# Performance work log

Hardware: AMD Instinct MI355X
Metric: run time of the kernel (lower is better)

Reference implementation:

```python
import jax, jax.numpy as jnp
import numpy as np

THETA_BASE = 10000.0


def rope(x):
    # x: [B, S, D], D even. Interleaved-pair rotary embedding.
    B, S, D = x.shape
    pos = jnp.arange(S, dtype=jnp.float32)                       # [S]
    p = jnp.arange(D // 2, dtype=jnp.float32)                    # p-1 in the torch code
    inv_freq = 1.0 / (THETA_BASE ** (2.0 * p / D))               # [D/2]
    theta = pos[:, None] * inv_freq[None, :]                     # [S, D/2]
    sin_t, cos_t = jnp.sin(theta), jnp.cos(theta)
    x1 = x[..., 0::2]                                            # [B, S, D/2]
    x2 = x[..., 1::2]
    r1 = x1 * cos_t - x2 * sin_t
    r2 = x1 * sin_t + x2 * cos_t
    return jnp.stack((r1, r2), axis=-1).reshape(B, S, D)


def setup_inputs() -> dict:
    key = jax.random.key(0)
    k_x, k_q, k_k, k_v = jax.random.split(key, 4)
    B, S, E, DH = 4, 4096, 1024, 64
    x = jax.random.normal(k_x, (B, S, E), dtype=jnp.float32)
    # causal lower-triangular mask (mask==0 positions are disallowed)
    mask = jnp.tril(jnp.ones((S, S), dtype=jnp.int32))
    W_Q = jax.random.uniform(k_q, (E, DH), dtype=jnp.float32)
    W_K = jax.random.uniform(k_k, (E, DH), dtype=jnp.float32)
    W_V = jax.random.uniform(k_v, (E, DH), dtype=jnp.float32)
    return {"x": x, "mask": mask, "W_Q": W_Q, "W_K": W_K, "W_V": W_V}


def reference(x, mask, W_Q, W_K, W_V):
    d_h = W_Q.shape[1]
    Q = x @ W_Q                                                  # [B, S, d_h]
    K = x @ W_K
    V = x @ W_V
    Q, K = rope(Q), rope(K)
    scores = jnp.einsum('bqd,bkd->bqk', Q, K) / jnp.sqrt(jnp.float32(d_h))
    masked = jnp.where(mask == 0, -jnp.inf, scores)              # broadcast [S,S] -> [B,S,S]
    attn = jax.nn.softmax(masked, axis=-1)
    return jnp.einsum('bqk,bkd->bqd', attn, V)
```

## Files before the change

### kernel.cpp

```cpp
#include <hip/hip_runtime.h>

typedef short short8  __attribute__((ext_vector_type(8)));
typedef short short4v __attribute__((ext_vector_type(4)));
typedef float f32x4   __attribute__((ext_vector_type(4)));

#define NB 4
#define NS 4096
#define NE 1024
#define ND 64

__device__ __forceinline__ short f2bf(float f) {
    unsigned u = __builtin_bit_cast(unsigned, f);
    u = (u + 0x7FFFu + ((u >> 16) & 1u)) >> 16;
    return (short)u;
}
__device__ __forceinline__ float bf2f(short s) {
    unsigned u = ((unsigned)(unsigned short)s) << 16;
    return __builtin_bit_cast(float, u);
}

__global__ void prep_wt(const float* __restrict__ WQ, const float* __restrict__ WK,
                        const float* __restrict__ WV,
                        short* __restrict__ wtp_hi, short* __restrict__ wtp_lo) {
    int idx = blockIdx.x * 256 + threadIdx.x;
    if (idx >= 192 * NE) return;
    int n = idx >> 10, k = idx & (NE - 1);
    int sel = n >> 6, d = n & 63;
    const float* W = (sel == 0) ? WQ : (sel == 1 ? WK : WV);
    float v = W[k * ND + d];
    if (sel == 0) v *= 0.125f;
    short hi = f2bf(v);
    short lo = f2bf(v - bf2f(hi));
    int off = ((k >> 5) * 12 + (n >> 4)) * 512 + ((k & 31) >> 3) * 128 + (n & 15) * 8 + (k & 7);
    wtp_hi[off] = hi;
    wtp_lo[off] = lo;
}

__global__ __launch_bounds__(256, 2) void proj_rope(
        const float* __restrict__ x,
        const short* __restrict__ wtp_hi, const short* __restrict__ wtp_lo,
        short* __restrict__ qhi, short* __restrict__ qlo,
        short* __restrict__ khi, short* __restrict__ klo,
        short* __restrict__ vtb) {
    __shared__ short Xh[32 * 64], Xl[32 * 64];
    const int tid = threadIdx.x;
    const int w = tid >> 6, lane = tid & 63;
    const int g = lane >> 4, cl = lane & 15;
    const int rb = blockIdx.x << 5;
    const int c0 = w * 48;

    f32x4 acc[2][3];
    #pragma unroll
    for (int i = 0; i < 2; ++i)
        #pragma unroll
        for (int j = 0; j < 3; ++j) acc[i][j] = (f32x4){0.f, 0.f, 0.f, 0.f};

    const int srow = tid >> 3, skc = tid & 7;
    const float* xs0 = x + (size_t)(rb + srow) * NE + (skc << 3);
    const int swoff = srow * 64 + ((skc ^ (srow & 7)) << 3);

    const short* bph = wtp_hi + (size_t)(c0 >> 4) * 512 + (lane << 3);
    const short* bpl = wtp_lo + (size_t)(c0 >> 4) * 512 + (lane << 3);

    float4 xr0, xr1;
    short8 b0[6], b1[6];

#define LOADXR(kk) { xr0 = *(const float4*)(xs0 + (kk)); \
                     xr1 = *(const float4*)(xs0 + (kk) + 4); }
#define LOADB(Bs, kk) {                                                      \
        const int ko = ((kk) >> 5) * 6144;                                   \
        _Pragma("unroll")                                                    \
        for (int ct = 0; ct < 3; ++ct) {                                     \
            Bs[ct * 2]     = *(const short8*)(bph + ko + ct * 512);          \
            Bs[ct * 2 + 1] = *(const short8*)(bpl + ko + ct * 512);          \
        } }
#define HALF(h, Bs) {                                                        \
        _Pragma("unroll")                                                    \
        for (int rt = 0; rt < 2; ++rt) {                                     \
            const int R = (rt << 4) + cl;                                    \
            const int ro = R * 64 + ((((h) * 4 + g) ^ (R & 7)) << 3);        \
            short8 ah = *(const short8*)(Xh + ro);                           \
            short8 al = *(const short8*)(Xl + ro);                           \
            _Pragma("unroll")                                                \
            for (int ct = 0; ct < 3; ++ct) {                                 \
                acc[rt][ct] = __builtin_amdgcn_mfma_f32_16x16x32_bf16(ah, Bs[ct*2],   acc[rt][ct], 0, 0, 0); \
                acc[rt][ct] = __builtin_amdgcn_mfma_f32_16x16x32_bf16(ah, Bs[ct*2+1], acc[rt][ct], 0, 0, 0); \
                acc[rt][ct] = __builtin_amdgcn_mfma_f32_16x16x32_bf16(al, Bs[ct*2],   acc[rt][ct], 0, 0, 0); \
            }                                                                \
        } }

    LOADXR(0);
    LOADB(b0, 0);

    #pragma unroll 1
    for (int k0 = 0; k0 < NE; k0 += 64) {
        short8 h8, l8;
        {
            float vv[8] = {xr0.x, xr0.y, xr0.z, xr0.w, xr1.x, xr1.y, xr1.z, xr1.w};
            #pragma unroll
            for (int q = 0; q < 8; ++q) {
                short h = f2bf(vv[q]);
                h8[q] = h;
                l8[q] = f2bf(vv[q] - bf2f(h));
            }
        }
        __syncthreads();
        *(short8*)(Xh + swoff) = h8;
        *(short8*)(Xl + swoff) = l8;
        if (k0 + 64 < NE) LOADXR(k0 + 64);
        LOADB(b1, k0 + 32);
        __syncthreads();
        HALF(0, b0);
        if (k0 + 64 < NE) LOADB(b0, k0 + 64);
        HALF(1, b1);
    }
#undef LOADXR
#undef LOADB
#undef HALF

    #pragma unroll
    for (int rt = 0; rt < 2; ++rt) {
        #pragma unroll
        for (int ct = 0; ct < 3; ++ct) {
            int c = c0 + (ct << 4) + cl;
            #pragma unroll
            for (int r = 0; r < 4; ++r) {
                int row = rb + (rt << 4) + (g << 2) + r;
                int s = row & (NS - 1);
                int b = row >> 12;
                float val = acc[rt][ct][r];
                if (c < 128) {
                    int d = c & 63;
                    int p = d >> 1;
                    float freq = exp2f(-(float)p * 0.41524101186091903f);
                    float theta = (float)s * freq;
                    float sn = sinf(theta), cs = cosf(theta);
                    float partner = __shfl_xor(val, 1);
                    float rot = (c & 1) ? fmaf(partner, sn, val * cs)
                                        : fmaf(-partner, sn, val * cs);
                    short hi = f2bf(rot);
                    short lo = f2bf(rot - bf2f(hi));
                    int off = row * ND + d;
                    if (c < 64) { qhi[off] = hi; qlo[off] = lo; }
                    else        { khi[off] = hi; klo[off] = lo; }
                } else {
                    int d = c - 128;
                    vtb[(b << 18) + ((s >> 5) << 11) + (d << 5) + (s & 31)] = f2bf(val);
                }
            }
        }
    }
}

__global__ __launch_bounds__(256) void kv_pack(short* __restrict__ khi,
                                               short* __restrict__ klo,
                                               short* __restrict__ vtb) {
    __shared__ short Xh[2048], Xl[2048], Vl[2048];
    const int tid = threadIdx.x;
    const size_t base = (size_t)blockIdx.x * 2048;
    *(short8*)(Xh + tid * 8) = *(const short8*)(khi + base + tid * 8);
    *(short8*)(Xl + tid * 8) = *(const short8*)(klo + base + tid * 8);
    *(short8*)(Vl + tid * 8) = *(const short8*)(vtb + base + tid * 8);
    __syncthreads();
    const int ci = (tid >> 7) & 1, hf = (tid >> 6) & 1, ln = tid & 63;
    const int srcK = (ci * 16 + (ln & 15)) * 64 + hf * 32 + (ln >> 4) * 8;
    short8 okh = *(const short8*)(Xh + srcK);
    short8 okl = *(const short8*)(Xl + srcK);
    const int dt = (tid >> 6) & 3;
    const int srcV = (dt * 16 + (ln & 15)) * 32 + (ln >> 4) * 8;
    short8 ov = *(const short8*)(Vl + srcV);
    *(short8*)(khi + base + tid * 8) = okh;
    *(short8*)(klo + base + tid * 8) = okl;
    *(short8*)(vtb + base + tid * 8) = ov;
}

__global__ __launch_bounds__(256, 4) void attn_fused(
        const short* __restrict__ qhi, const short* __restrict__ qlo,
        const short* __restrict__ kfph, const short* __restrict__ kfpl,
        const short* __restrict__ vfp, float* __restrict__ outp) {
    __shared__ short Ps[4][16][40];
    __shared__ float Co[4][16][66];
    __shared__ float Cm[4][16], Cls[4][16];
    const int tid = threadIdx.x;
    const int lane = tid & 63, w = tid >> 6;
    const int g = lane >> 4, cl = lane & 15;
    const int bid = blockIdx.x;
    const int b = (bid >> 1) & 3;
    const int t = 255 - (((bid >> 3) << 1) | (bid & 1));
    const int qw = t << 4;
    const int rowb = b << 12;

    short8 qh[2], ql[2];
    #pragma unroll
    for (int ks = 0; ks < 2; ++ks) {
        int off = ((rowb + qw + cl) << 6) + (ks << 5) + (g << 3);
        qh[ks] = *(const short8*)(qhi + off);
        ql[ks] = *(const short8*)(qlo + off);
    }

    f32x4 o[4];
    #pragma unroll
    for (int i = 0; i < 4; ++i) o[i] = (f32x4){0.f, 0.f, 0.f, 0.f};
    float m = -1e38f, lsp = 0.f;

    const int nkv = (t >> 1) + 1;
    const short* kbaseh = kfph + (size_t)(b << 7) * 2048 + (lane << 3);
    const short* kbasel = kfpl + (size_t)(b << 7) * 2048 + (lane << 3);
    const short* vbase  = vfp  + (size_t)(b << 7) * 2048 + (lane << 3);

    short8 kf[2][4];
    short8 vf[4];

#define LOADK(jj) {                                                          \
        _Pragma("unroll")                                                    \
        for (int ci = 0; ci < 2; ++ci) {                                     \
            const short* kh = kbaseh + (jj) * 2048 + ci * 1024;              \
            const short* kl = kbasel + (jj) * 2048 + ci * 1024;              \
            kf[ci][0] = *(const short8*)(kh);                                \
            kf[ci][1] = *(const short8*)(kh + 512);                          \
            kf[ci][2] = *(const short8*)(kl);                                \
            kf[ci][3] = *(const short8*)(kl + 512);                          \
        } }
#define LOADV(jj) {                                                          \
        _Pragma("unroll")                                                    \
        for (int dt = 0; dt < 4; ++dt)                                       \
            vf[dt] = *(const short8*)(vbase + (jj) * 2048 + dt * 512);       \
        }

    if (w < nkv) {
        LOADK(w); LOADV(w);
        #pragma unroll 1
        for (int j = w; j < nkv; j += 4) {
            f32x4 sc[2];
            #pragma unroll
            for (int ci = 0; ci < 2; ++ci) {
                f32x4 s = (f32x4){0.f, 0.f, 0.f, 0.f};
                s = __builtin_amdgcn_mfma_f32_16x16x32_bf16(kf[ci][0], qh[0], s, 0, 0, 0);
                s = __builtin_amdgcn_mfma_f32_16x16x32_bf16(kf[ci][1], qh[1], s, 0, 0, 0);
                s = __builtin_amdgcn_mfma_f32_16x16x32_bf16(kf[ci][0], ql[0], s, 0, 0, 0);
                s = __builtin_amdgcn_mfma_f32_16x16x32_bf16(kf[ci][1], ql[1], s, 0, 0, 0);
                s = __builtin_amdgcn_mfma_f32_16x16x32_bf16(kf[ci][2], qh[0], s, 0, 0, 0);
                s = __builtin_amdgcn_mfma_f32_16x16x32_bf16(kf[ci][3], qh[1], s, 0, 0, 0);
                sc[ci] = s;
            }
            const int jn = j + 4;
            if (jn < nkv) LOADK(jn);

            if (j == nkv - 1) {
                #pragma unroll
                for (int ci = 0; ci < 2; ++ci)
                    #pragma unroll
                    for (int r = 0; r < 4; ++r)
                        if ((j << 5) + (ci << 4) + (g << 2) + r > qw + cl) sc[ci][r] = -1e30f;
            }
            float pm = fmaxf(fmaxf(fmaxf(sc[0][0], sc[0][1]), fmaxf(sc[0][2], sc[0][3])),
                             fmaxf(fmaxf(sc[1][0], sc[1][1]), fmaxf(sc[1][2], sc[1][3])));
            pm = fmaxf(pm, __shfl_xor(pm, 16));
            pm = fmaxf(pm, __shfl_xor(pm, 32));
            const float mo = m;
            m = fmaxf(m, pm);
            const float rs = __expf(mo - m);
            float psum = 0.f;
            #pragma unroll
            for (int ci = 0; ci < 2; ++ci) {
                float p0 = __expf(sc[ci][0] - m), p1 = __expf(sc[ci][1] - m);
                float p2 = __expf(sc[ci][2] - m), p3 = __expf(sc[ci][3] - m);
                psum += (p0 + p1) + (p2 + p3);
                short4v pk;
                pk[0] = f2bf(p0); pk[1] = f2bf(p1); pk[2] = f2bf(p2); pk[3] = f2bf(p3);
                *(short4v*)(&Ps[w][cl][(ci << 4) + (g << 2)]) = pk;
            }
            lsp = lsp * rs + psum;
            if (__any(m > mo)) {
                float rs4[4];
                #pragma unroll
                for (int r = 0; r < 4; ++r) rs4[r] = __shfl(rs, (g << 2) + r);
                #pragma unroll
                for (int dt = 0; dt < 4; ++dt)
                    #pragma unroll
                    for (int r = 0; r < 4; ++r) o[dt][r] *= rs4[r];
            }
            short8 pa = *(short8*)(&Ps[w][cl][g << 3]);
            #pragma unroll
            for (int dt = 0; dt < 4; ++dt)
                o[dt] = __builtin_amdgcn_mfma_f32_16x16x32_bf16(pa, vf[dt], o[dt], 0, 0, 0);
            if (jn < nkv) LOADV(jn);
        }
    }
#undef LOADK
#undef LOADV

    lsp += __shfl_xor(lsp, 16);
    lsp += __shfl_xor(lsp, 32);
    if (g == 0) { Cm[w][cl] = m; Cls[w][cl] = lsp; }
    #pragma unroll
    for (int dt = 0; dt < 4; ++dt)
        #pragma unroll
        for (int r = 0; r < 4; ++r)
            Co[w][(g << 2) + r][(dt << 4) + cl] = o[dt][r];
    __syncthreads();

    if (w == 0) {
        #pragma unroll
        for (int r = 0; r < 4; ++r) {
            const int row = (g << 2) + r;
            float M = fmaxf(fmaxf(Cm[0][row], Cm[1][row]), fmaxf(Cm[2][row], Cm[3][row]));
            float e0 = __expf(Cm[0][row] - M), e1 = __expf(Cm[1][row] - M);
            float e2 = __expf(Cm[2][row] - M), e3 = __expf(Cm[3][row] - M);
            float L = Cls[0][row] * e0 + Cls[1][row] * e1 + Cls[2][row] * e2 + Cls[3][row] * e3;
            float inv = 1.f / L;
            #pragma unroll
            for (int dt = 0; dt < 4; ++dt) {
                int d = (dt << 4) + cl;
                float O = Co[0][row][d] * e0 + Co[1][row][d] * e1
                        + Co[2][row][d] * e2 + Co[3][row][d] * e3;
                outp[(rowb + qw + row) * ND + d] = O * inv;
            }
        }
    }
}

extern "C" void kernel_launch(void* const* d_in, const int* in_sizes, int n_in,
                              void* d_out, int out_size, void* d_ws, size_t ws_size,
                              hipStream_t stream) {
    const float* x  = (const float*)d_in[0];
    const float* WQ = (const float*)d_in[2];
    const float* WK = (const float*)d_in[3];
    const float* WV = (const float*)d_in[4];

    const size_t need = 786432u + 5u * 2097152u;
    if (ws_size < need) return;

    char* ws = (char*)d_ws;
    short* wtph = (short*)(ws);
    short* wtpl = (short*)(ws + 393216);
    short* qhi  = (short*)(ws + 786432);
    short* qlo  = (short*)(ws + 786432 + 1 * 2097152);
    short* khi  = (short*)(ws + 786432 + 2 * 2097152);
    short* klo  = (short*)(ws + 786432 + 3 * 2097152);
    short* vtb  = (short*)(ws + 786432 + 4 * 2097152);

    prep_wt<<<768, 256, 0, stream>>>(WQ, WK, WV, wtph, wtpl);
    proj_rope<<<512, 256, 0, stream>>>(x, wtph, wtpl, qhi, qlo, khi, klo, vtb);
    kv_pack<<<512, 256, 0, stream>>>(khi, klo, vtb);
    attn_fused<<<1024, 256, 0, stream>>>(qhi, qlo, khi, klo, vtb, (float*)d_out);
}
```

Measured before the change: 82.09 us.

## Double-buffer X tile in projection kernel and halve rows per block

The projection kernel now double-buffers the converted X tile in shared memory. The next chunk is converted and stored while the current one feeds the MFMAs, which cuts the barriers per iteration from two to one, implemented as a custom LDS wait plus barrier. Row tile per block drops from 32 to 16, so the grid doubles to 1024 blocks and only half the threads stage X. This trades more parallelism and overlap for less weight reuse per block, so the weight-fragment loads per output row double.

```diff
diff --git a/kernel.cpp b/kernel.cpp
--- a/kernel.cpp
+++ b/kernel.cpp
@@ -18,6 +18,12 @@
     unsigned u = ((unsigned)(unsigned short)s) << 16;
     return __builtin_bit_cast(float, u);
 }
+
+#define LDS_BAR() do {                                               \
+        asm volatile("s_waitcnt lgkmcnt(0)" ::: "memory");           \
+        __builtin_amdgcn_s_barrier();                                \
+        __builtin_amdgcn_sched_barrier(0);                           \
+    } while (0)
 
 __global__ void prep_wt(const float* __restrict__ WQ, const float* __restrict__ WK,
                         const float* __restrict__ WV,
@@ -42,22 +48,20 @@
         short* __restrict__ qhi, short* __restrict__ qlo,
         short* __restrict__ khi, short* __restrict__ klo,
         short* __restrict__ vtb) {
-    __shared__ short Xh[32 * 64], Xl[32 * 64];
+    __shared__ short Xh[2][1024], Xl[2][1024];
     const int tid = threadIdx.x;
     const int w = tid >> 6, lane = tid & 63;
     const int g = lane >> 4, cl = lane & 15;
-    const int rb = blockIdx.x << 5;
+    const int rb = blockIdx.x << 4;
     const int c0 = w * 48;
 
-    f32x4 acc[2][3];
-    #pragma unroll
-    for (int i = 0; i < 2; ++i)
-        #pragma unroll
-        for (int j = 0; j < 3; ++j) acc[i][j] = (f32x4){0.f, 0.f, 0.f, 0.f};
+    f32x4 acc[3];
+    acc[0] = acc[1] = acc[2] = (f32x4){0.f, 0.f, 0.f, 0.f};
 
     const int srow = tid >> 3, skc = tid & 7;
     const float* xs0 = x + (size_t)(rb + srow) * NE + (skc << 3);
     const int swoff = srow * 64 + ((skc ^ (srow & 7)) << 3);
+    const bool stager = (tid < 128);
 
     const short* bph = wtp_hi + (size_t)(c0 >> 4) * 512 + (lane << 3);
     const short* bpl = wtp_lo + (size_t)(c0 >> 4) * 512 + (lane << 3);
@@ -74,79 +78,79 @@
             Bs[ct * 2]     = *(const short8*)(bph + ko + ct * 512);          \
             Bs[ct * 2 + 1] = *(const short8*)(bpl + ko + ct * 512);          \
         } }
-#define HALF(h, Bs) {                                                        \
-        _Pragma("unroll")                                                    \
-        for (int rt = 0; rt < 2; ++rt) {                                     \
-            const int R = (rt << 4) + cl;                                    \
-            const int ro = R * 64 + ((((h) * 4 + g) ^ (R & 7)) << 3);        \
-            short8 ah = *(const short8*)(Xh + ro);                           \
-            short8 al = *(const short8*)(Xl + ro);                           \
-            _Pragma("unroll")                                                \
-            for (int ct = 0; ct < 3; ++ct) {                                 \
-                acc[rt][ct] = __builtin_amdgcn_mfma_f32_16x16x32_bf16(ah, Bs[ct*2],   acc[rt][ct], 0, 0, 0); \
-                acc[rt][ct] = __builtin_amdgcn_mfma_f32_16x16x32_bf16(ah, Bs[ct*2+1], acc[rt][ct], 0, 0, 0); \
-                acc[rt][ct] = __builtin_amdgcn_mfma_f32_16x16x32_bf16(al, Bs[ct*2],   acc[rt][ct], 0, 0, 0); \
-            }                                                                \
+#define CONVW(buf) if (stager) {                                             \
+        float vv[8] = {xr0.x, xr0.y, xr0.z, xr0.w, xr1.x, xr1.y, xr1.z, xr1.w}; \
+        short8 h8, l8;                                                       \
+        _Pragma("unroll")                                                    \
+        for (int q = 0; q < 8; ++q) {                                        \
+            short h = f2bf(vv[q]);                                           \
+            h8[q] = h;                                                       \
+            l8[q] = f2bf(vv[q] - bf2f(h));                                   \
+        }                                                                    \
+        *(short8*)(Xh[buf] + swoff) = h8;                                    \
+        *(short8*)(Xl[buf] + swoff) = l8;                                    \
+    }
+#define HALF(buf, h, Bs) {                                                   \
+        const int ro = cl * 64 + ((((h) * 4 + g) ^ (cl & 7)) << 3);          \
+        short8 ah = *(const short8*)(Xh[buf] + ro);                          \
+        short8 al = *(const short8*)(Xl[buf] + ro);                          \
+        _Pragma("unroll")                                                    \
+        for (int ct = 0; ct < 3; ++ct) {                                     \
+            acc[ct] = __builtin_amdgcn_mfma_f32_16x16x32_bf16(ah, Bs[ct*2],   acc[ct], 0, 0, 0); \
+            acc[ct] = __builtin_amdgcn_mfma_f32_16x16x32_bf16(ah, Bs[ct*2+1], acc[ct], 0, 0, 0); \
+            acc[ct] = __builtin_amdgcn_mfma_f32_16x16x32_bf16(al, Bs[ct*2],   acc[ct], 0, 0, 0); \
         } }
 
-    LOADXR(0);
+    if (stager) LOADXR(0);
+    CONVW(0);
+    if (stager) LOADXR(64);
     LOADB(b0, 0);
+    __syncthreads();
 
     #pragma unroll 1
     for (int k0 = 0; k0 < NE; k0 += 64) {
-        short8 h8, l8;
-        {
-            float vv[8] = {xr0.x, xr0.y, xr0.z, xr0.w, xr1.x, xr1.y, xr1.z, xr1.w};
-            #pragma unroll
-            for (int q = 0; q < 8; ++q) {
-                short h = f2bf(vv[q]);
-                h8[q] = h;
-                l8[q] = f2bf(vv[q] - bf2f(h));
-            }
-        }
-        __syncthreads();
-        *(short8*)(Xh + swoff) = h8;
-        *(short8*)(Xl + swoff) = l8;
-        if (k0 + 64 < NE) LOADXR(k0 + 64);
+        const int cur = (k0 >> 6) & 1, nxt = cur ^ 1;
+        if (k0 + 64 < NE) {
+            CONVW(nxt);
+            if (stager && k0 + 128 < NE) LOADXR(k0 + 128);
+        }
         LOADB(b1, k0 + 32);
-        __syncthreads();
-        HALF(0, b0);
+        HALF(cur, 0, b0);
         if (k0 + 64 < NE) LOADB(b0, k0 + 64);
-        HALF(1, b1);
+        HALF(cur, 1, b1);
+        LDS_BAR();
     }
 #undef LOADXR
 #undef LOADB
+#undef CONVW
 #undef HALF
 
     #pragma unroll
-    for (int rt = 0; rt < 2; ++rt) {
+    for (int ct = 0; ct < 3; ++ct) {
+        int c = c0 + (ct << 4) + cl;
         #pragma unroll
-        for (int ct = 0; ct < 3; ++ct) {
-            int c = c0 + (ct << 4) + cl;
-            #pragma unroll
-            for (int r = 0; r < 4; ++r) {
-                int row = rb + (rt << 4) + (g << 2) + r;
-                int s = row & (NS - 1);
-                int b = row >> 12;
-                float val = acc[rt][ct][r];
-                if (c < 128) {
-                    int d = c & 63;
-                    int p = d >> 1;
-                    float freq = exp2f(-(float)p * 0.41524101186091903f);
-                    float theta = (float)s * freq;
-                    float sn = sinf(theta), cs = cosf(theta);
-                    float partner = __shfl_xor(val, 1);
-                    float rot = (c & 1) ? fmaf(partner, sn, val * cs)
-                                        : fmaf(-partner, sn, val * cs);
-                    short hi = f2bf(rot);
-                    short lo = f2bf(rot - bf2f(hi));
-                    int off = row * ND + d;
-                    if (c < 64) { qhi[off] = hi; qlo[off] = lo; }
-                    else        { khi[off] = hi; klo[off] = lo; }
-                } else {
-                    int d = c - 128;
-                    vtb[(b << 18) + ((s >> 5) << 11) + (d << 5) + (s & 31)] = f2bf(val);
-                }
+        for (int r = 0; r < 4; ++r) {
+            int row = rb + (g << 2) + r;
+            int s = row & (NS - 1);
+            int b = row >> 12;
+            float val = acc[ct][r];
+            if (c < 128) {
+                int d = c & 63;
+                int p = d >> 1;
+                float freq = exp2f(-(float)p * 0.41524101186091903f);
+                float theta = (float)s * freq;
+                float sn = sinf(theta), cs = cosf(theta);
+                float partner = __shfl_xor(val, 1);
+                float rot = (c & 1) ? fmaf(partner, sn, val * cs)
+                                    : fmaf(-partner, sn, val * cs);
+                short hi = f2bf(rot);
+                short lo = f2bf(rot - bf2f(hi));
+                int off = row * ND + d;
+                if (c < 64) { qhi[off] = hi; qlo[off] = lo; }
+                else        { khi[off] = hi; klo[off] = lo; }
+            } else {
+                int d = c - 128;
+                vtb[(b << 18) + ((s >> 5) << 11) + (d << 5) + (s & 31)] = f2bf(val);
             }
         }
     }
@@ -341,7 +345,7 @@
     short* vtb  = (short*)(ws + 786432 + 4 * 2097152);
 
     prep_wt<<<768, 256, 0, stream>>>(WQ, WK, WV, wtph, wtpl);
-    proj_rope<<<512, 256, 0, stream>>>(x, wtph, wtpl, qhi, qlo, khi, klo, vtb);
+    proj_rope<<<1024, 256, 0, stream>>>(x, wtph, wtpl, qhi, qlo, khi, klo, vtb);
     kv_pack<<<512, 256, 0, stream>>>(khi, klo, vtb);
     attn_fused<<<1024, 256, 0, stream>>>(qhi, qlo, khi, klo, vtb, (float*)d_out);
 }
```

Result: slower. 88.63 us (+8.0%).
